# Optimization experiments

Hardware: AMD Instinct MI355X
Metric: run time of the kernel (lower is better)

Reference implementation:

```python
import jax, jax.numpy as jnp
import numpy as np

DIM = 128
NUM_HEADS = 4
WINDOW = (7, 7)


def _rel_pos_index(wh, ww):
    h = jnp.arange(wh)
    w = jnp.arange(ww)
    idx = jnp.stack(jnp.meshgrid(w, h, indexing='ij'))  # (2, wh, ww)
    flat = idx.reshape(2, -1)                           # (2, n)
    rel = flat[:, :, None] - flat[:, None, :]           # (2, n, n)
    rel = jnp.transpose(rel, (1, 2, 0))                 # (n, n, 2)
    rel = rel.at[:, :, 0].add(wh - 1)
    rel = rel.at[:, :, 1].add(ww - 1)
    rel = rel.at[:, :, 0].multiply(2 * ww - 1)
    return jnp.sum(rel, -1)                             # (n, n)


def setup_inputs() -> dict:
    key = jax.random.key(0)
    ks = jax.random.split(key, 7)
    batch, n, c = 4096, WINDOW[0] * WINDOW[1], DIM
    nw = 64  # windows per image; batch % nw == 0
    return {
        'inputs': jax.random.normal(ks[0], (batch, n, c), jnp.float32),
        'mask': jax.random.normal(ks[1], (nw, n, n), jnp.float32),
        'qkv_w': jax.random.normal(ks[2], (c, 3 * c), jnp.float32) * 0.02,
        'qkv_b': jax.random.normal(ks[3], (3 * c,), jnp.float32) * 0.02,
        'proj_w': jax.random.normal(ks[4], (c, c), jnp.float32) * 0.02,
        'proj_b': jax.random.normal(ks[5], (c,), jnp.float32) * 0.02,
        'rpbt': jax.random.normal(ks[6], ((2 * WINDOW[0] - 1) * (2 * WINDOW[1] - 1), NUM_HEADS), jnp.float32) * 0.02,
    }


def reference(inputs, mask, qkv_w, qkv_b, proj_w, proj_b, rpbt):
    batch, n, c = inputs.shape
    head_dim = DIM // NUM_HEADS
    qkv = inputs @ qkv_w + qkv_b                       # (B, n, 3C)
    qkv = qkv.reshape(batch, n, 3, NUM_HEADS, head_dim)
    qkv = jnp.transpose(qkv, (2, 0, 3, 1, 4))          # (3, B, H, n, d)
    q, k, v = qkv[0], qkv[1], qkv[2]
    q = q * head_dim ** -0.5
    att = jnp.einsum('bhqd,bhkd->bhqk', q, k)          # (B, H, n, n)
    rel_idx = _rel_pos_index(*WINDOW).reshape(-1)
    bias = rpbt[rel_idx].reshape(n, n, NUM_HEADS)      # gather
    att = att + jnp.transpose(bias, (2, 0, 1))[None]   # (B, H, n, n)
    nw = mask.shape[0]
    att = att.reshape(batch // nw, nw, NUM_HEADS, n, n)
    att = att + mask[None, :, None]
    att = att.reshape(batch, NUM_HEADS, n, n)
    att = jax.nn.softmax(att, axis=-1)
    x = jnp.einsum('bhqk,bhkd->bhqd', att, v)          # (B, H, n, d)
    x = jnp.transpose(x, (0, 2, 1, 3)).reshape(batch, n, c)
    return x @ proj_w + proj_b
```

## Files before the change

kernel.cpp:

```cpp
#include <hip/hip_runtime.h>

typedef __bf16 bf16x8 __attribute__((ext_vector_type(8)));
typedef float f32x4 __attribute__((ext_vector_type(4)));
typedef float f32x16 __attribute__((ext_vector_type(16)));
typedef unsigned short us4 __attribute__((ext_vector_type(4)));
typedef unsigned int u32x2 __attribute__((ext_vector_type(2)));

#define SCALE 0.17677669529663687f

__device__ __forceinline__ unsigned short f2bf(float f) {
    __bf16 h = (__bf16)f;
    return __builtin_bit_cast(unsigned short, h);
}
__device__ __forceinline__ unsigned pk2(float lo, float hi) {
    return (unsigned)f2bf(lo) | ((unsigned)f2bf(hi) << 16);
}
__device__ __forceinline__ us4 pack4(float a, float b, float c, float d) {
    us4 r; r[0] = f2bf(a); r[1] = f2bf(b); r[2] = f2bf(c); r[3] = f2bf(d); return r;
}

__global__ void wa_prep(const float* __restrict__ qkv_w, const float* __restrict__ proj_w,
                        const float* __restrict__ rpbt, const float* __restrict__ mask,
                        unsigned short* __restrict__ wq2, unsigned short* __restrict__ wp2,
                        float* __restrict__ tab, int use_bm) {
    int idx = blockIdx.x * 256 + threadIdx.x;
    if (idx < 49152) {
        int c2 = idx / 3072, rem = idx % 3072;
        int n = rem >> 3, j = rem & 7;
        int k = c2 * 8 + j;
        float v = qkv_w[k * 384 + n];
        if (n < 128) v *= SCALE;
        wq2[idx] = f2bf(v);
    } else if (idx < 65536) {
        int t = idx - 49152;
        int c2 = t >> 10, rem = t & 1023;
        int n = rem >> 3, j = rem & 7;
        int k = c2 * 8 + j;
        wp2[t] = f2bf(proj_w[k * 128 + n]);
    } else {
        int j = idx - 65536;
        if (use_bm) {
            if (j < 64 * 4 * 49 * 64) {
                int k = j & 63; int t = j >> 6; int q = t % 49; t /= 49;
                int h = t & 3, w = t >> 2;
                float v = 0.f;
                if (k < 49) {
                    int rel = (q / 7 - k / 7 + 6) * 13 + (q % 7 - k % 7 + 6);
                    v = rpbt[rel * 4 + h] + mask[w * 2401 + q * 49 + k];
                }
                tab[j] = v;
            }
        } else {
            if (j < 4 * 49 * 64) {
                int k = j & 63; int t = j >> 6; int q = t % 49; int h = t / 49;
                float v = 0.f;
                if (k < 49) {
                    int rel = (q / 7 - k / 7 + 6) * 13 + (q % 7 - k % 7 + 6);
                    v = rpbt[rel * 4 + h];
                }
                tab[j] = v;
            }
        }
    }
}

__global__ __launch_bounds__(512, 6) void wa_main(
    const float* __restrict__ x, const float* __restrict__ mask,
    const float* __restrict__ qkv_b, const float* __restrict__ proj_b,
    const unsigned short* __restrict__ wq2, const unsigned short* __restrict__ wp2,
    const float* __restrict__ tab, int use_bm, float* __restrict__ out)
{
    __shared__ __align__(16) char smem[49152];
    char* const Qs = smem;
    char* const Ks = smem + 16384;
    char* const Cx = smem + 32768;

    const int tid  = threadIdx.x;
    const int wv   = tid >> 6;
    const int lane = tid & 63;
    const int l31  = lane & 31;
    const int hi   = lane >> 5;
    const int b    = blockIdx.x;

    {
        const float* xp = x + (size_t)b * 6272;
        for (int i = tid; i < 1568; i += 512) {
            int row = i >> 5;
            int cb  = (i & 31) * 8;
            f32x4 v = *reinterpret_cast<const f32x4*>(xp + i * 4);
            *reinterpret_cast<us4*>(Cx + row * 256 + (cb ^ ((row & 7) << 4))) =
                pack4(v[0], v[1], v[2], v[3]);
        }
        us4 z = (us4)(unsigned short)0;
        for (int i = tid; i < 480; i += 512) {
            int row = 49 + (i >> 5);
            int cb  = (i & 31) * 8;
            *reinterpret_cast<us4*>(Cx + row * 256 + (cb ^ ((row & 7) << 4))) = z;
        }
    }
    __syncthreads();

    {
        const int rt = wv >> 2, c4 = wv & 3;
        const int arow = rt * 32 + l31;

        #pragma unroll 1
        for (int t = 0; t < 2; ++t) {
            const int colg = t * 128 + c4 * 32 + l31;
            f32x16 acc;
            #pragma unroll
            for (int i = 0; i < 16; ++i) acc[i] = 0.f;
            #pragma unroll
            for (int kk = 0; kk < 8; ++kk) {
                bf16x8 af = *reinterpret_cast<const bf16x8*>(
                    Cx + arow * 256 + ((kk * 32 + hi * 16) ^ ((arow & 7) << 4)));
                bf16x8 bw = *reinterpret_cast<const bf16x8*>(
                    wq2 + ((kk * 2 + hi) * 384 + colg) * 8);
                acc = __builtin_amdgcn_mfma_f32_32x32x16_bf16(af, bw, acc, 0, 0, 0);
            }
            float bv = qkv_b[colg] * (t == 0 ? SCALE : 1.0f);
            char* dst = (t == 0 ? Qs : Ks) + c4 * 4096;
            #pragma unroll
            for (int r = 0; r < 16; ++r) {
                int row = rt * 32 + (r & 3) + 8 * (r >> 2) + 4 * hi;
                *reinterpret_cast<unsigned short*>(
                    dst + row * 64 + ((l31 * 2) ^ ((row & 3) << 4))) = f2bf(acc[r] + bv);
            }
        }
        f32x16 avv;
        #pragma unroll
        for (int i = 0; i < 16; ++i) avv[i] = 0.f;
        {
            const int colg = 256 + c4 * 32 + l31;
            #pragma unroll
            for (int kk = 0; kk < 8; ++kk) {
                bf16x8 af = *reinterpret_cast<const bf16x8*>(
                    Cx + arow * 256 + ((kk * 32 + hi * 16) ^ ((arow & 7) << 4)));
                bf16x8 bw = *reinterpret_cast<const bf16x8*>(
                    wq2 + ((kk * 2 + hi) * 384 + colg) * 8);
                avv = __builtin_amdgcn_mfma_f32_32x32x16_bf16(af, bw, avv, 0, 0, 0);
            }
        }
        __syncthreads();
        {
            float bvv = qkv_b[256 + c4 * 32 + l31];
            #pragma unroll
            for (int g = 0; g < 4; ++g) {
                int tok0 = rt * 32 + 8 * g + 4 * hi;
                u32x2 pv;
                pv[0] = pk2(avv[g * 4 + 0] + bvv, avv[g * 4 + 1] + bvv);
                pv[1] = pk2(avv[g * 4 + 2] + bvv, avv[g * 4 + 3] + bvv);
                *reinterpret_cast<u32x2*>(
                    Cx + c4 * 4096 + l31 * 128 + ((tok0 * 2) ^ ((l31 & 7) << 4))) = pv;
            }
        }
    }
    __syncthreads();

    {
        const int h2 = wv >> 1, qh = wv & 1;
        const int q  = qh * 32 + l31;

        f32x16 S0, S1;
        #pragma unroll
        for (int i = 0; i < 16; ++i) { S0[i] = 0.f; S1[i] = 0.f; }
        #pragma unroll
        for (int s = 0; s < 2; ++s) {
            const int off = s * 32 + hi * 16;
            bf16x8 qf = *reinterpret_cast<const bf16x8*>(
                Qs + h2 * 4096 + q * 64 + (off ^ ((q & 3) << 4)));
            bf16x8 k0 = *reinterpret_cast<const bf16x8*>(
                Ks + h2 * 4096 + l31 * 64 + (off ^ ((l31 & 3) << 4)));
            bf16x8 k1 = *reinterpret_cast<const bf16x8*>(
                Ks + h2 * 4096 + (32 + l31) * 64 + (off ^ ((l31 & 3) << 4)));
            S0 = __builtin_amdgcn_mfma_f32_32x32x16_bf16(k0, qf, S0, 0, 0, 0);
            S1 = __builtin_amdgcn_mfma_f32_32x32x16_bf16(k1, qf, S1, 0, 0, 0);
        }

        const float* tp = tab + (size_t)(use_bm ? ((b & 63) * 4 + h2) : h2) * (49 * 64);
        const float* mp = mask + (size_t)(b & 63) * 2401;
        const bool qv = q < 49;
        const int qc = qv ? q : 48;
        const float* trow = tp + qc * 64;

        float mx = -1e30f;
        #pragma unroll
        for (int g = 0; g < 4; ++g) {
            f32x4 t0 = *reinterpret_cast<const f32x4*>(trow + g * 8 + hi * 4);
            f32x4 t1 = *reinterpret_cast<const f32x4*>(trow + 32 + g * 8 + hi * 4);
            #pragma unroll
            for (int e = 0; e < 4; ++e) {
                float v0 = S0[g * 4 + e] + t0[e];
                float v1 = S1[g * 4 + e] + t1[e];
                if (!use_bm) {
                    v0 += mp[qc * 49 + g * 8 + hi * 4 + e];
                    int k1i = 32 + g * 8 + hi * 4 + e;
                    if (k1i < 49) v1 += mp[qc * 49 + k1i];
                }
                v0 = qv ? v0 : -1e30f;
                v1 = (qv && (g * 8 + hi * 4 + e) < 17) ? v1 : -1e30f;
                S0[g * 4 + e] = v0;  mx = fmaxf(mx, v0);
                S1[g * 4 + e] = v1;  mx = fmaxf(mx, v1);
            }
        }
        mx = fmaxf(mx, __shfl_xor(mx, 32));
        float sum = 0.f;
        #pragma unroll
        for (int i = 0; i < 16; ++i) {
            float e0 = __expf(S0[i] - mx);
            float e1 = __expf(S1[i] - mx);
            S0[i] = e0; S1[i] = e1;
            sum += e0 + e1;
        }
        sum += __shfl_xor(sum, 32);
        float ri = __builtin_amdgcn_rcpf(sum);

        unsigned pp[2][4][2];
        #pragma unroll
        for (int g = 0; g < 4; ++g) {
            pp[0][g][0] = pk2(S0[g * 4 + 0] * ri, S0[g * 4 + 1] * ri);
            pp[0][g][1] = pk2(S0[g * 4 + 2] * ri, S0[g * 4 + 3] * ri);
            pp[1][g][0] = pk2(S1[g * 4 + 0] * ri, S1[g * 4 + 1] * ri);
            pp[1][g][1] = pk2(S1[g * 4 + 2] * ri, S1[g * 4 + 3] * ri);
        }

        f32x16 X;
        #pragma unroll
        for (int i = 0; i < 16; ++i) X[i] = 0.f;
        const bool lo = (hi == 0);
        #pragma unroll
        for (int s = 0; s < 4; ++s) {
            const int kt = s >> 1, u = (s & 1) * 2;
            unsigned a0 = pp[kt][u][0],     a1 = pp[kt][u][1];
            unsigned b0 = pp[kt][u + 1][0], b1 = pp[kt][u + 1][1];
            unsigned sa0 = (unsigned)__shfl_xor((int)a0, 32);
            unsigned sa1 = (unsigned)__shfl_xor((int)a1, 32);
            unsigned sb0 = (unsigned)__shfl_xor((int)b0, 32);
            unsigned sb1 = (unsigned)__shfl_xor((int)b1, 32);
            union { unsigned u4[4]; bf16x8 v; } A;
            A.u4[0] = lo ? a0  : sb0;
            A.u4[1] = lo ? a1  : sb1;
            A.u4[2] = lo ? sa0 : b0;
            A.u4[3] = lo ? sa1 : b1;
            bf16x8 Bf = *reinterpret_cast<const bf16x8*>(
                Cx + h2 * 4096 + l31 * 128 + ((s * 32 + hi * 16) ^ ((l31 & 7) << 4)));
            X = __builtin_amdgcn_mfma_f32_32x32x16_bf16(A.v, Bf, X, 0, 0, 0);
        }
        __syncthreads();
        #pragma unroll
        for (int r = 0; r < 16; ++r) {
            int row = qh * 32 + (r & 3) + 8 * (r >> 2) + 4 * hi;
            int col = h2 * 32 + l31;
            *reinterpret_cast<unsigned short*>(
                Qs + row * 256 + ((col * 2) ^ ((row & 7) << 4))) = f2bf(X[r]);
        }
    }
    __syncthreads();

    {
        const int prt = wv >> 2, pct = wv & 3;
        const int xrow = prt * 32 + l31;
        f32x16 o;
        #pragma unroll
        for (int i = 0; i < 16; ++i) o[i] = 0.f;
        #pragma unroll
        for (int kk = 0; kk < 8; ++kk) {
            bf16x8 af = *reinterpret_cast<const bf16x8*>(
                Qs + xrow * 256 + ((kk * 32 + hi * 16) ^ ((xrow & 7) << 4)));
            bf16x8 bw = *reinterpret_cast<const bf16x8*>(
                wp2 + ((kk * 2 + hi) * 128 + pct * 32 + l31) * 8);
            o = __builtin_amdgcn_mfma_f32_32x32x16_bf16(af, bw, o, 0, 0, 0);
        }
        float pb = proj_b[pct * 32 + l31];
        float* op = out + (size_t)b * 6272 + pct * 32 + l31;
        #pragma unroll
        for (int r = 0; r < 16; ++r) {
            int row = prt * 32 + (r & 3) + 8 * (r >> 2) + 4 * hi;
            if (row < 49) op[row * 128] = o[r] + pb;
        }
    }
}

extern "C" void kernel_launch(void* const* d_in, const int* in_sizes, int n_in,
                              void* d_out, int out_size, void* d_ws, size_t ws_size,
                              hipStream_t stream) {
    const float* x      = (const float*)d_in[0];
    const float* mask   = (const float*)d_in[1];
    const float* qkv_w  = (const float*)d_in[2];
    const float* qkv_b  = (const float*)d_in[3];
    const float* proj_w = (const float*)d_in[4];
    const float* proj_b = (const float*)d_in[5];
    const float* rpbt   = (const float*)d_in[6];
    float* out = (float*)d_out;

    unsigned short* wq2 = (unsigned short*)d_ws;
    unsigned short* wp2 = (unsigned short*)((char*)d_ws + 98304);
    float*          tab = (float*)((char*)d_ws + 131072);

    const size_t needed_big = 131072 + (size_t)64 * 4 * 49 * 64 * 4;
    int use_bm = (ws_size >= needed_big) ? 1 : 0;
    int total  = 65536 + (use_bm ? 64 * 4 * 49 * 64 : 4 * 49 * 64);

    wa_prep<<<(total + 255) / 256, 256, 0, stream>>>(qkv_w, proj_w, rpbt, mask, wq2, wp2, tab, use_bm);
    wa_main<<<4096, 512, 0, stream>>>(x, mask, qkv_b, proj_b, wq2, wp2, tab, use_bm, out);
}
```

Baseline: 110.7 us.

## Reorder barriers to overlap V transpose with scores, use exp2 softmax

Q and K are now stored row-major with a 256-byte stride instead of per-head 4 KB blocks, so the V transpose write into the x buffer can move after the projection barrier and overlap with the QK^T and softmax phase. The barrier before the PV matmul now covers both V visibility and the later Q overwrite, which removes one block-wide sync. Log2(e) is folded into the Q weights, Q bias and bias/mask table so softmax can use exp2 in place of __expf. This adds a dependence on barrier placement for correctness and slightly changes rounding.

```diff
diff --git a/kernel.cpp b/kernel.cpp
--- a/kernel.cpp
+++ b/kernel.cpp
@@ -7,6 +7,7 @@
 typedef unsigned int u32x2 __attribute__((ext_vector_type(2)));
 
 #define SCALE 0.17677669529663687f
+#define LOG2E 1.4426950408889634f
 
 __device__ __forceinline__ unsigned short f2bf(float f) {
     __bf16 h = (__bf16)f;
@@ -29,7 +30,7 @@
         int n = rem >> 3, j = rem & 7;
         int k = c2 * 8 + j;
         float v = qkv_w[k * 384 + n];
-        if (n < 128) v *= SCALE;
+        if (n < 128) v *= SCALE * LOG2E;
         wq2[idx] = f2bf(v);
     } else if (idx < 65536) {
         int t = idx - 49152;
@@ -46,7 +47,7 @@
                 float v = 0.f;
                 if (k < 49) {
                     int rel = (q / 7 - k / 7 + 6) * 13 + (q % 7 - k % 7 + 6);
-                    v = rpbt[rel * 4 + h] + mask[w * 2401 + q * 49 + k];
+                    v = (rpbt[rel * 4 + h] + mask[w * 2401 + q * 49 + k]) * LOG2E;
                 }
                 tab[j] = v;
             }
@@ -56,7 +57,7 @@
                 float v = 0.f;
                 if (k < 49) {
                     int rel = (q / 7 - k / 7 + 6) * 13 + (q % 7 - k % 7 + 6);
-                    v = rpbt[rel * 4 + h];
+                    v = rpbt[rel * 4 + h] * LOG2E;
                 }
                 tab[j] = v;
             }
@@ -100,8 +101,11 @@
     }
     __syncthreads();
 
+    f32x16 avv;
+    int p1_rt, p1_c4;
     {
         const int rt = wv >> 2, c4 = wv & 3;
+        p1_rt = rt; p1_c4 = c4;
         const int arow = rt * 32 + l31;
 
         #pragma unroll 1
@@ -118,16 +122,16 @@
                     wq2 + ((kk * 2 + hi) * 384 + colg) * 8);
                 acc = __builtin_amdgcn_mfma_f32_32x32x16_bf16(af, bw, acc, 0, 0, 0);
             }
-            float bv = qkv_b[colg] * (t == 0 ? SCALE : 1.0f);
-            char* dst = (t == 0 ? Qs : Ks) + c4 * 4096;
+            float bv = qkv_b[colg] * (t == 0 ? SCALE * LOG2E : 1.0f);
+            char* dst = (t == 0 ? Qs : Ks);
+            const int colb = (c4 * 32 + l31) * 2;
             #pragma unroll
             for (int r = 0; r < 16; ++r) {
                 int row = rt * 32 + (r & 3) + 8 * (r >> 2) + 4 * hi;
                 *reinterpret_cast<unsigned short*>(
-                    dst + row * 64 + ((l31 * 2) ^ ((row & 3) << 4))) = f2bf(acc[r] + bv);
-            }
-        }
-        f32x16 avv;
+                    dst + row * 256 + (colb ^ ((row & 7) << 4))) = f2bf(acc[r] + bv);
+            }
+        }
         #pragma unroll
         for (int i = 0; i < 16; ++i) avv[i] = 0.f;
         {
@@ -141,21 +145,21 @@
                 avv = __builtin_amdgcn_mfma_f32_32x32x16_bf16(af, bw, avv, 0, 0, 0);
             }
         }
-        __syncthreads();
-        {
-            float bvv = qkv_b[256 + c4 * 32 + l31];
-            #pragma unroll
-            for (int g = 0; g < 4; ++g) {
-                int tok0 = rt * 32 + 8 * g + 4 * hi;
-                u32x2 pv;
-                pv[0] = pk2(avv[g * 4 + 0] + bvv, avv[g * 4 + 1] + bvv);
-                pv[1] = pk2(avv[g * 4 + 2] + bvv, avv[g * 4 + 3] + bvv);
-                *reinterpret_cast<u32x2*>(
-                    Cx + c4 * 4096 + l31 * 128 + ((tok0 * 2) ^ ((l31 & 7) << 4))) = pv;
-            }
-        }
     }
     __syncthreads();
+
+    {
+        float bvv = qkv_b[256 + p1_c4 * 32 + l31];
+        #pragma unroll
+        for (int g = 0; g < 4; ++g) {
+            int tok0 = p1_rt * 32 + 8 * g + 4 * hi;
+            u32x2 pv;
+            pv[0] = pk2(avv[g * 4 + 0] + bvv, avv[g * 4 + 1] + bvv);
+            pv[1] = pk2(avv[g * 4 + 2] + bvv, avv[g * 4 + 3] + bvv);
+            *reinterpret_cast<u32x2*>(
+                Cx + p1_c4 * 4096 + l31 * 128 + ((tok0 * 2) ^ ((l31 & 7) << 4))) = pv;
+        }
+    }
 
     {
         const int h2 = wv >> 1, qh = wv & 1;
@@ -166,13 +170,13 @@
         for (int i = 0; i < 16; ++i) { S0[i] = 0.f; S1[i] = 0.f; }
         #pragma unroll
         for (int s = 0; s < 2; ++s) {
-            const int off = s * 32 + hi * 16;
+            const int off = h2 * 64 + s * 32 + hi * 16;
             bf16x8 qf = *reinterpret_cast<const bf16x8*>(
-                Qs + h2 * 4096 + q * 64 + (off ^ ((q & 3) << 4)));
+                Qs + q * 256 + (off ^ ((q & 7) << 4)));
             bf16x8 k0 = *reinterpret_cast<const bf16x8*>(
-                Ks + h2 * 4096 + l31 * 64 + (off ^ ((l31 & 3) << 4)));
+                Ks + l31 * 256 + (off ^ ((l31 & 7) << 4)));
             bf16x8 k1 = *reinterpret_cast<const bf16x8*>(
-                Ks + h2 * 4096 + (32 + l31) * 64 + (off ^ ((l31 & 3) << 4)));
+                Ks + (32 + l31) * 256 + (off ^ ((l31 & 7) << 4)));
             S0 = __builtin_amdgcn_mfma_f32_32x32x16_bf16(k0, qf, S0, 0, 0, 0);
             S1 = __builtin_amdgcn_mfma_f32_32x32x16_bf16(k1, qf, S1, 0, 0, 0);
         }
@@ -193,9 +197,9 @@
                 float v0 = S0[g * 4 + e] + t0[e];
                 float v1 = S1[g * 4 + e] + t1[e];
                 if (!use_bm) {
-                    v0 += mp[qc * 49 + g * 8 + hi * 4 + e];
+                    v0 += mp[qc * 49 + g * 8 + hi * 4 + e] * LOG2E;
                     int k1i = 32 + g * 8 + hi * 4 + e;
-                    if (k1i < 49) v1 += mp[qc * 49 + k1i];
+                    if (k1i < 49) v1 += mp[qc * 49 + k1i] * LOG2E;
                 }
                 v0 = qv ? v0 : -1e30f;
                 v1 = (qv && (g * 8 + hi * 4 + e) < 17) ? v1 : -1e30f;
@@ -207,8 +211,8 @@
         float sum = 0.f;
         #pragma unroll
         for (int i = 0; i < 16; ++i) {
-            float e0 = __expf(S0[i] - mx);
-            float e1 = __expf(S1[i] - mx);
+            float e0 = exp2f(S0[i] - mx);
+            float e1 = exp2f(S1[i] - mx);
             S0[i] = e0; S1[i] = e1;
             sum += e0 + e1;
         }
@@ -223,6 +227,8 @@
             pp[1][g][0] = pk2(S1[g * 4 + 0] * ri, S1[g * 4 + 1] * ri);
             pp[1][g][1] = pk2(S1[g * 4 + 2] * ri, S1[g * 4 + 3] * ri);
         }
+
+        __syncthreads();
 
         f32x16 X;
         #pragma unroll
@@ -246,7 +252,6 @@
                 Cx + h2 * 4096 + l31 * 128 + ((s * 32 + hi * 16) ^ ((l31 & 7) << 4)));
             X = __builtin_amdgcn_mfma_f32_32x32x16_bf16(A.v, Bf, X, 0, 0, 0);
         }
-        __syncthreads();
         #pragma unroll
         for (int r = 0; r < 16; ++r) {
             int row = qh * 32 + (r & 3) + 8 * (r >> 2) + 4 * hi;
```

Result: slower. 184.4 us (+66.6%).
